# Kernel optimization log

Measured on AMD Instinct MI355X. Metric: run time of the kernel, lower is better.

## Reference

```python
import jax, jax.numpy as jnp
import numpy as np

B, S, D, H, L = 8, 2048, 512, 8, 5
DK = D // H
SP = S - L + 1  # number of local windows


def setup_inputs() -> dict:
    key = jax.random.key(0)
    ks = jax.random.split(key, 5)
    scale = 1.0 / np.sqrt(D).astype(np.float32)
    return {
        "query": jax.random.normal(ks[0], (B, S, D), dtype=jnp.float32),
        "key": jax.random.normal(ks[1], (B, S, D), dtype=jnp.float32),
        "value": jax.random.normal(ks[2], (B, S, D), dtype=jnp.float32),
        "W0": jax.random.normal(ks[3], (D, D), dtype=jnp.float32) * scale,
        "b0": jnp.zeros((D,), dtype=jnp.float32),
        "Wout": jax.random.normal(ks[4], (D, D), dtype=jnp.float32) * scale,
        "bout": jnp.zeros((D,), dtype=jnp.float32),
    }


def _local_agg(x, weighted):
    # x: (B, S, D). Sliding-window aggregation over windows of length L.
    # scores[b, t, s] = <x[b, t+L-1], x[b, s]> / sqrt(D)  -- per the source:
    # matmul(x[:, L-1:], x^T) / sqrt(d_model)
    scores = jnp.einsum("btd,bsd->bts", x[:, L - 1:], x) / (float(D) ** 0.5)
    idx = jnp.arange(SP)[:, None] + jnp.arange(L)[None, :]  # (SP, L)
    # per-window softmax over the L local scores
    w = jax.nn.softmax(jnp.take_along_axis(scores, idx[None, :, :], axis=-1), axis=-1)  # (B, SP, L)
    win = x[:, idx]  # (B, SP, L, D) gathered windows
    if weighted:
        win = w[..., None] * win
    return jnp.sum(win, axis=2)  # (B, SP, D)


def reference(query, key, value, W0, b0, Wout, bout):
    # Bug-faithful: the source overwrites the weighted query with the raw
    # windows (`query = q_list`), so query windows are summed UNweighted;
    # key windows use the local softmax weights.
    q = _local_agg(query, weighted=False)  # (B, SP, D)
    k = _local_agg(key, weighted=True)     # (B, SP, D)
    v = value[:, L - 1:] @ W0 + b0         # linears[0], aligned to SP positions

    def heads(t):  # (B, SP, D) -> (B, H, SP, DK)
        return t.reshape(t.shape[0], t.shape[1], H, DK).transpose(0, 2, 1, 3)

    qh, kh, vh = heads(q), heads(k), heads(v)
    att = jax.nn.softmax(jnp.einsum("bhtd,bhsd->bhts", qh, kh) / (float(DK) ** 0.5), axis=-1)
    x = jnp.einsum("bhts,bhsd->bhtd", att, vh)  # (B, H, SP, DK)
    x = x.transpose(0, 2, 1, 3).reshape(q.shape[0], SP, D)
    return x @ Wout + bout  # linears[-1]
```

## Files before the change

### kernel.cpp

```cpp
#include <hip/hip_runtime.h>
#include <hip/hip_bf16.h>
#include <hip/hip_fp16.h>

#define B_ 8
#define S_ 2048
#define D_ 512
#define H_ 8
#define L_ 5
#define DK_ 64
#define SP_ 2044
#define SPAD_ 2048

typedef _Float16 f16_t;
typedef _Float16 f16x4 __attribute__((ext_vector_type(4)));
typedef _Float16 f16x8 __attribute__((ext_vector_type(8)));
typedef __fp16 fp16x2_b __attribute__((ext_vector_type(2)));
typedef float f32x4 __attribute__((ext_vector_type(4)));
typedef float f32x16 __attribute__((ext_vector_type(16)));
typedef unsigned int u32;

static __device__ __forceinline__ f32x4 mfma16(f16x8 a, f16x8 b, f32x4 c) {
    return __builtin_amdgcn_mfma_f32_16x16x32_f16(a, b, c, 0, 0, 0);
}
static __device__ __forceinline__ f32x16 mfma32(f16x8 a, f16x8 b, f32x16 c) {
    return __builtin_amdgcn_mfma_f32_32x32x16_f16(a, b, c, 0, 0, 0);
}

union U32H2 { u32 u; fp16x2_b h; };
union FRAG { uint4 u; f16x8 f; };

#define LGKMBAR() do {                                 \
    __builtin_amdgcn_sched_barrier(0);                 \
    asm volatile("s_waitcnt lgkmcnt(0)");              \
    __builtin_amdgcn_s_barrier();                      \
    __builtin_amdgcn_sched_barrier(0);                 \
} while (0)

static __device__ __forceinline__ void swap32(u32 a, u32 b, u32& r0, u32& r1, int hi) {
#if __has_builtin(__builtin_amdgcn_permlane32_swap)
    auto r = __builtin_amdgcn_permlane32_swap(a, b, false, false);
    r0 = r[0]; r1 = r[1];
#else
    u32 t = __shfl_xor(hi ? a : b, 32, 64);
    r0 = hi ? t : a;
    r1 = hi ? b : t;
#endif
}

__global__ __launch_bounds__(256) void k_convert_w(
    const float* __restrict__ W0, const float* __restrict__ Wout,
    f16_t* __restrict__ WT0, f16_t* __restrict__ WT1) {
    int idx = blockIdx.x * 256 + threadIdx.x;
    int which = idx >> 18;
    int e = idx & 0x3FFFF;
    int k = e >> 9, n = e & 511;
    const float* W = which ? Wout : W0;
    f16_t* WT = which ? WT1 : WT0;
    WT[n * 512 + k] = (f16_t)W[k * 512 + n];
}

__global__ __launch_bounds__(256) void k_prep(
    const float* __restrict__ Qin, const float* __restrict__ Kin,
    f16_t* __restrict__ qh, f16_t* __restrict__ kh) {
    const int lane = threadIdx.x & 63;
    const int wid = threadIdx.x >> 6;
    const int gw = blockIdx.x * 4 + wid;
    const int b = gw >> 9;
    const int t0 = (gw & 511) * 4;
    const float* qb = Qin + (size_t)b * S_ * D_;
    const float* kb = Kin + (size_t)b * S_ * D_;
    const int d0 = lane * 8;

    float kr[8][8];
#pragma unroll
    for (int r = 0; r < 8; r++) {
        int row = t0 + r; row = row < 2047 ? row : 2047;
        const float4* kp = (const float4*)(kb + (size_t)row * D_ + d0);
        float4 ka = kp[0], kc = kp[1];
        kr[r][0] = ka.x; kr[r][1] = ka.y; kr[r][2] = ka.z; kr[r][3] = ka.w;
        kr[r][4] = kc.x; kr[r][5] = kc.y; kr[r][6] = kc.z; kr[r][7] = kc.w;
    }
    float qs[4][8];
#pragma unroll
    for (int w = 0; w < 4; w++)
#pragma unroll
        for (int e = 0; e < 8; e++) qs[w][e] = 0.f;
#pragma unroll
    for (int r = 0; r < 8; r++) {
        int row = t0 + r; row = row < 2047 ? row : 2047;
        const float4* qp = (const float4*)(qb + (size_t)row * D_ + d0);
        float4 a = qp[0], c = qp[1];
        float qe[8] = {a.x, a.y, a.z, a.w, c.x, c.y, c.z, c.w};
#pragma unroll
        for (int w = 0; w < 4; w++) {
            if (w <= r && r <= w + 4) {
#pragma unroll
                for (int e = 0; e < 8; e++) qs[w][e] += qe[e];
            }
        }
    }
    float dp[4][5];
#pragma unroll
    for (int w = 0; w < 4; w++) {
#pragma unroll
        for (int l = 0; l < 5; l++) {
            float d = 0.f;
#pragma unroll
            for (int e = 0; e < 8; e++) d += kr[w + 4][e] * kr[w + l][e];
            dp[w][l] = d;
        }
    }
#pragma unroll
    for (int m = 32; m; m >>= 1) {
#pragma unroll
        for (int w = 0; w < 4; w++)
#pragma unroll
            for (int l = 0; l < 5; l++) dp[w][l] += __shfl_xor(dp[w][l], m, 64);
    }
    const float sc = 0.044194173824159216f;
    const float qscale = 0.125f * 1.4426950408889634f;
    const int h = d0 >> 6, dk = d0 & 63;
#pragma unroll
    for (int w = 0; w < 4; w++) {
        float mx = dp[w][0];
#pragma unroll
        for (int l = 1; l < 5; l++) mx = fmaxf(mx, dp[w][l]);
        float wgt[5], sum = 0.f;
#pragma unroll
        for (int l = 0; l < 5; l++) { wgt[l] = __expf((dp[w][l] - mx) * sc); sum += wgt[l]; }
        float inv = 1.f / sum;
        f16x8 qpk, kpk;
#pragma unroll
        for (int e = 0; e < 8; e++) {
            float v = 0.f;
#pragma unroll
            for (int l = 0; l < 5; l++) v += wgt[l] * kr[w + l][e];
            kpk[e] = (f16_t)(v * inv);
            qpk[e] = (f16_t)(qs[w][e] * qscale);
        }
        const size_t ob = ((size_t)(b * H_ + h) * SPAD_ + (t0 + w)) * DK_ + dk;
        *(f16x8*)(qh + ob) = qpk;
        *(f16x8*)(kh + ob) = kpk;
    }
}

template <int MODE>
__global__ __launch_bounds__(256) void k_gemm(
    const void* __restrict__ Aptr, const f16_t* __restrict__ WT,
    const float* __restrict__ bias, void* __restrict__ Cptr) {
    __shared__ alignas(16) char smem[40960];
    const int tid = threadIdx.x, lane = tid & 63, wid = tid >> 6;
    const int mt = blockIdx.x >> 2, nt = blockIdx.x & 3;
    const int m0 = mt * 128, n0 = nt * 128;
    const int l15 = lane & 15, lg = lane >> 4;
    f32x4 acc[2][8] = {};

    const float* a0src = nullptr;
    const f16_t* a1src0 = nullptr, *a1src1 = nullptr;
    if (MODE == 0) {
        const float* A = (const float*)Aptr;
        int r = tid >> 1, cb = (tid & 1) * 16;
        int rp = m0 + r, b = rp >> 11, t = rp & 2047;
        int vrow = t + 4; vrow = vrow < 2047 ? vrow : 2047;
        a0src = A + ((size_t)b * 2048 + vrow) * 512 + cb;
    } else {
        const f16_t* A = (const f16_t*)Aptr;
        int r0 = tid >> 2, off0 = (tid & 3) * 8;
        int r1 = (tid + 256) >> 2;
        a1src0 = A + (size_t)(m0 + r0) * 512 + off0;
        a1src1 = A + (size_t)(m0 + r1) * 512 + off0;
    }
    const int bnl0 = tid >> 2, bko0 = (tid & 3) * 8;
    const int bnl1 = (tid + 256) >> 2;
    const f16_t* bsrc0 = WT + (size_t)(n0 + bnl0) * 512 + bko0;
    const f16_t* bsrc1 = WT + (size_t)(n0 + bnl1) * 512 + bko0;

    float4 fa[4];
    uint4 ua0, ua1, ub0, ub1;
    if (MODE == 0) {
#pragma unroll
        for (int j = 0; j < 4; j++) fa[j] = *(const float4*)(a0src + j * 4);
    } else {
        ua0 = *(const uint4*)a1src0;
        ua1 = *(const uint4*)a1src1;
    }
    ub0 = *(const uint4*)bsrc0;
    ub1 = *(const uint4*)bsrc1;

    for (int kt = 0; kt < 16; ++kt) {
        const int cur = kt & 1;
        f16_t (*Asm)[40] = (f16_t(*)[40])(smem + cur * 10240);
        f16_t (*Bsm)[40] = (f16_t(*)[40])(smem + 20480 + cur * 10240);
        if (MODE == 0) {
            int r = tid >> 1, cb = (tid & 1) * 16;
            f16x8 p0, p1;
            p0[0] = (f16_t)fa[0].x; p0[1] = (f16_t)fa[0].y; p0[2] = (f16_t)fa[0].z; p0[3] = (f16_t)fa[0].w;
            p0[4] = (f16_t)fa[1].x; p0[5] = (f16_t)fa[1].y; p0[6] = (f16_t)fa[1].z; p0[7] = (f16_t)fa[1].w;
            p1[0] = (f16_t)fa[2].x; p1[1] = (f16_t)fa[2].y; p1[2] = (f16_t)fa[2].z; p1[3] = (f16_t)fa[2].w;
            p1[4] = (f16_t)fa[3].x; p1[5] = (f16_t)fa[3].y; p1[6] = (f16_t)fa[3].z; p1[7] = (f16_t)fa[3].w;
            *(f16x8*)&Asm[r][cb] = p0;
            *(f16x8*)&Asm[r][cb + 8] = p1;
        } else {
            int r0 = tid >> 2, r1 = (tid + 256) >> 2, off = (tid & 3) * 8;
            *(uint4*)&Asm[r0][off] = ua0;
            *(uint4*)&Asm[r1][off] = ua1;
        }
        *(uint4*)&Bsm[bnl0][bko0] = ub0;
        *(uint4*)&Bsm[bnl1][bko0] = ub1;
        if (kt < 15) {
            const int k0n = (kt + 1) * 32;
            if (MODE == 0) {
#pragma unroll
                for (int j = 0; j < 4; j++) fa[j] = *(const float4*)(a0src + k0n + j * 4);
            } else {
                ua0 = *(const uint4*)(a1src0 + k0n);
                ua1 = *(const uint4*)(a1src1 + k0n);
            }
            ub0 = *(const uint4*)(bsrc0 + k0n);
            ub1 = *(const uint4*)(bsrc1 + k0n);
        }
        __syncthreads();
        f16x8 af[2], bfr[8];
#pragma unroll
        for (int i = 0; i < 2; i++) af[i] = *(const f16x8*)&Asm[wid * 32 + i * 16 + l15][lg * 8];
#pragma unroll
        for (int c = 0; c < 8; c++) bfr[c] = *(const f16x8*)&Bsm[c * 16 + l15][lg * 8];
        __builtin_amdgcn_s_setprio(1);
#pragma unroll
        for (int i = 0; i < 2; i++) {
#pragma unroll
            for (int c = 0; c < 8; c++) acc[i][c] = mfma16(af[i], bfr[c], acc[i][c]);
        }
        __builtin_amdgcn_s_setprio(0);
    }

    if (MODE == 0) {
        __syncthreads();
        f16_t (*Csm)[136] = (f16_t(*)[136])smem;
#pragma unroll
        for (int i = 0; i < 2; i++) {
#pragma unroll
            for (int c = 0; c < 8; c++) {
                int col = n0 + c * 16 + l15;
                float bv = bias[col];
                f16x4 pk;
#pragma unroll
                for (int r = 0; r < 4; r++) pk[r] = (f16_t)(acc[i][c][r] + bv);
                *(f16x4*)&Csm[c * 16 + l15][wid * 32 + i * 16 + lg * 4] = pk;
            }
        }
        __syncthreads();
        const int b = m0 >> 11, t0 = m0 & 2047;
        const int cl = tid >> 1, mo = (tid & 1) * 64;
        const int h = (n0 + cl) >> 6, dk = (n0 + cl) & 63;
        f16_t* dst = (f16_t*)Cptr + ((size_t)(b * H_ + h) * DK_ + dk) * SPAD_ + t0 + mo;
#pragma unroll
        for (int j = 0; j < 8; j++)
            *(uint4*)(dst + j * 8) = *(const uint4*)&Csm[cl][mo + j * 8];
    } else {
#pragma unroll
        for (int i = 0; i < 2; i++) {
#pragma unroll
            for (int c = 0; c < 8; c++) {
#pragma unroll
                for (int r = 0; r < 4; r++) {
                    int row = m0 + wid * 32 + i * 16 + lg * 4 + r;
                    int col = n0 + c * 16 + l15;
                    float v = acc[i][c][r] + bias[col];
                    int b = row >> 11, t = row & 2047;
                    if (t < SP_) {
                        float* outp = (float*)Cptr;
                        outp[((size_t)b * SP_ + t) * 512 + col] = v;
                    }
                }
            }
        }
    }
}

__global__ __launch_bounds__(256, 2) void k_attn(
    const f16_t* __restrict__ qh, const f16_t* __restrict__ kh,
    const f16_t* __restrict__ vhT, f16_t* __restrict__ xatt) {
    __shared__ alignas(16) f16_t Ksm[2][64][68];
    __shared__ alignas(16) f16_t Vsm[2][64][68];
    const int tid = threadIdx.x, lane = tid & 63, wid = tid >> 6;
    const int l31 = lane & 31, hi = lane >> 5, hi8 = hi * 8;
    const int vb = ((blockIdx.x & 7) << 6) | (blockIdx.x >> 3);
    const int bh = vb >> 3, qt = vb & 7;
    const f16_t* Q = qh + (size_t)bh * SPAD_ * DK_;
    const f16_t* K = kh + (size_t)bh * SPAD_ * DK_;
    const f16_t* VT = vhT + (size_t)bh * DK_ * SPAD_;
    const int qw = qt * 256 + wid * 64;

    f16x8 qf[2][4];
#pragma unroll
    for (int qg = 0; qg < 2; qg++)
#pragma unroll
        for (int kf = 0; kf < 4; kf++)
            qf[qg][kf] = *(const f16x8*)(Q + (size_t)(qw + qg * 32 + l31) * DK_ + kf * 16 + hi8);

    f32x16 cinit;
#pragma unroll
    for (int i = 0; i < 16; i++) cinit[i] = -12.f;

    f32x16 acc[2][2] = {};
    float rsa[2] = {0.f, 0.f}, rsb[2] = {0.f, 0.f};
    u32 pk[2][2][8];
    U32H2 one2; one2.u = 0x3C003C00u;

    const int sr = tid >> 3, so = (tid & 7) * 8;
    const f16_t* kg0 = K + (size_t)sr * DK_ + so;
    const f16_t* kg1 = K + (size_t)(sr + 32) * DK_ + so;
    const f16_t* vg0 = VT + (size_t)sr * SPAD_ + so;
    const f16_t* vg1 = VT + (size_t)(sr + 32) * SPAD_ + so;

    uint4 rk0 = *(const uint4*)kg0;
    uint4 rk1 = *(const uint4*)kg1;
    uint4 rv0 = *(const uint4*)vg0;
    uint4 rv1 = *(const uint4*)vg1;

    for (int t = 0; t < 32; ++t) {
        const int cur = t & 1;
        *(uint4*)&Ksm[cur][sr][so]      = rk0;
        *(uint4*)&Ksm[cur][sr + 32][so] = rk1;
        *(uint4*)&Vsm[cur][sr][so]      = rv0;
        *(uint4*)&Vsm[cur][sr + 32][so] = rv1;
        if (t < 31) {
            const int nxt = (t + 1) << 6;
            rk0 = *(const uint4*)(kg0 + (size_t)nxt * DK_);
            rk1 = *(const uint4*)(kg1 + (size_t)nxt * DK_);
            rv0 = *(const uint4*)(vg0 + nxt);
            rv1 = *(const uint4*)(vg1 + nxt);
        }
        LGKMBAR();

#pragma unroll
        for (int kr = 0; kr < 2; ++kr) {
            f32x16 sv0 = cinit, sv1 = cinit;
            __builtin_amdgcn_s_setprio(1);
#pragma unroll
            for (int kf = 0; kf < 4; ++kf) {
                f16x8 a = *(const f16x8*)&Ksm[cur][kr * 32 + l31][kf * 16 + hi8];
                sv0 = mfma32(a, qf[0][kf], sv0);
                sv1 = mfma32(a, qf[1][kf], sv1);
            }
            __builtin_amdgcn_s_setprio(0);
            if (t == 31 && kr == 1) {
#pragma unroll
                for (int r = 12; r < 16; ++r) {
                    sv0[r] = hi ? -1e30f : sv0[r];
                    sv1[r] = hi ? -1e30f : sv1[r];
                }
            }
#pragma unroll
            for (int j = 0; j < 8; ++j) {
                float a0 = __builtin_amdgcn_exp2f(sv0[2 * j]);
                float a1 = __builtin_amdgcn_exp2f(sv0[2 * j + 1]);
                U32H2 c0; c0.h = __builtin_amdgcn_cvt_pkrtz(a0, a1);
                pk[0][kr][j] = c0.u;
                float b0 = __builtin_amdgcn_exp2f(sv1[2 * j]);
                float b1 = __builtin_amdgcn_exp2f(sv1[2 * j + 1]);
                U32H2 c1; c1.h = __builtin_amdgcn_cvt_pkrtz(b0, b1);
                pk[1][kr][j] = c1.u;
#if __has_builtin(__builtin_amdgcn_fdot2)
                if (j & 1) {
                    rsb[0] = __builtin_amdgcn_fdot2(c0.h, one2.h, rsb[0], false);
                    rsb[1] = __builtin_amdgcn_fdot2(c1.h, one2.h, rsb[1], false);
                } else {
                    rsa[0] = __builtin_amdgcn_fdot2(c0.h, one2.h, rsa[0], false);
                    rsa[1] = __builtin_amdgcn_fdot2(c1.h, one2.h, rsa[1], false);
                }
#else
                if (j & 1) { rsb[0] += a0 + a1; rsb[1] += b0 + b1; }
                else       { rsa[0] += a0 + a1; rsa[1] += b0 + b1; }
#endif
            }
        }

#pragma unroll
        for (int kc = 0; kc < 4; ++kc) {
            const int kr = kc >> 1, al = (kc & 1) * 4;
            FRAG p0, p1;
            {
                u32 m0, m1, m2, m3;
                swap32(pk[0][kr][al],     pk[0][kr][al + 2], m0, m2, hi);
                swap32(pk[0][kr][al + 1], pk[0][kr][al + 3], m1, m3, hi);
                p0.u = make_uint4(m0, m1, m2, m3);
                swap32(pk[1][kr][al],     pk[1][kr][al + 2], m0, m2, hi);
                swap32(pk[1][kr][al + 1], pk[1][kr][al + 3], m1, m3, hi);
                p1.u = make_uint4(m0, m1, m2, m3);
            }
            __builtin_amdgcn_s_setprio(1);
#pragma unroll
            for (int dc = 0; dc < 2; ++dc) {
                f16x8 v = *(const f16x8*)&Vsm[cur][dc * 32 + l31][kc * 16 + hi8];
                acc[0][dc] = mfma32(v, p0.f, acc[0][dc]);
                acc[1][dc] = mfma32(v, p1.f, acc[1][dc]);
            }
            __builtin_amdgcn_s_setprio(0);
        }
    }

    float rs0 = rsa[0] + rsb[0];
    float rs1 = rsa[1] + rsb[1];
    rs0 += __shfl_xor(rs0, 32, 64);
    rs1 += __shfl_xor(rs1, 32, 64);
    const float inv[2] = {1.f / rs0, 1.f / rs1};

    __syncthreads();
    f16_t (*Osm)[68] = (f16_t(*)[68])&Ksm[0][0][0];
#pragma unroll
    for (int qg = 0; qg < 2; ++qg) {
        const int row = wid * 64 + qg * 32 + l31;
#pragma unroll
        for (int dc = 0; dc < 2; ++dc) {
#pragma unroll
            for (int p = 0; p < 8; ++p) {
                float e0 = acc[qg][dc][2 * p] * inv[qg];
                float e1 = acc[qg][dc][2 * p + 1] * inv[qg];
                U32H2 c; c.h = __builtin_amdgcn_cvt_pkrtz(e0, e1);
                const int d = dc * 32 + 2 * (p & 1) + 8 * (p >> 1) + 4 * hi;
                *(u32*)&Osm[row][d] = c.u;
            }
        }
    }
    __syncthreads();
    const int b = bh >> 3, hh = bh & 7;
#pragma unroll
    for (int ps = 0; ps < 8; ++ps) {
        const int row = wid * 64 + ps * 8 + (lane >> 3);
        const int dco = (lane & 7) * 8;
        uint4 v = *(const uint4*)&Osm[row][dco];
        f16_t* dst = xatt + ((size_t)b * SPAD_ + qt * 256 + row) * D_ + hh * DK_ + dco;
        *(uint4*)dst = v;
    }
}

extern "C" void kernel_launch(void* const* d_in, const int* in_sizes, int n_in,
                              void* d_out, int out_size, void* d_ws, size_t ws_size,
                              hipStream_t stream) {
    const float* query = (const float*)d_in[0];
    const float* key   = (const float*)d_in[1];
    const float* value = (const float*)d_in[2];
    const float* W0    = (const float*)d_in[3];
    const float* b0    = (const float*)d_in[4];
    const float* Wout  = (const float*)d_in[5];
    const float* bout  = (const float*)d_in[6];
    float* out = (float*)d_out;

    char* w = (char*)d_ws;
    const size_t SZ = (size_t)B_ * H_ * SPAD_ * DK_ * sizeof(f16_t);
    f16_t* qh   = (f16_t*)w; w += SZ;
    f16_t* kh   = (f16_t*)w; w += SZ;
    f16_t* vhT  = (f16_t*)w; w += SZ;
    f16_t* xatt = (f16_t*)w; w += SZ;
    f16_t* WT0  = (f16_t*)w; w += (size_t)512 * 512 * sizeof(f16_t);
    f16_t* WT1  = (f16_t*)w; w += (size_t)512 * 512 * sizeof(f16_t);

    k_convert_w<<<2048, 256, 0, stream>>>(W0, Wout, WT0, WT1);
    k_prep<<<1024, 256, 0, stream>>>(query, key, qh, kh);
    k_gemm<0><<<512, 256, 0, stream>>>((const void*)value, WT0, b0, (void*)vhT);
    k_attn<<<512, 256, 0, stream>>>(qh, kh, vhT, xatt);
    k_gemm<1><<<512, 256, 0, stream>>>((const void*)xatt, WT1, bout, (void*)out);
}
```

Before: 150.9 us.

## Merge value GEMM with local-window prep into one launch; tile weight transpose

Combines the V projection GEMM and the query/key sliding-window prep into a single kernel. The first 512 blocks run the GEMM and the remaining 1024 run the prep, so the two independent stages overlap and one launch disappears. The weight transpose/convert kernel now stages 64x64 tiles through shared memory, giving coalesced reads and vectorized writes in place of strided scattered writes. The combined kernel uses the larger shared-memory footprint for every block, including prep blocks that do not need it, which may lower their occupancy.

```diff
diff --git a/kernel.cpp b/kernel.cpp
--- a/kernel.cpp
+++ b/kernel.cpp
@@ -50,104 +50,210 @@
 __global__ __launch_bounds__(256) void k_convert_w(
     const float* __restrict__ W0, const float* __restrict__ Wout,
     f16_t* __restrict__ WT0, f16_t* __restrict__ WT1) {
-    int idx = blockIdx.x * 256 + threadIdx.x;
-    int which = idx >> 18;
-    int e = idx & 0x3FFFF;
-    int k = e >> 9, n = e & 511;
+    __shared__ float T[64][65];
+    const int bid = blockIdx.x;
+    const int which = bid >> 6;
+    const int tile = bid & 63;
+    const int K0 = (tile >> 3) * 64, N0 = (tile & 7) * 64;
     const float* W = which ? Wout : W0;
     f16_t* WT = which ? WT1 : WT0;
-    WT[n * 512 + k] = (f16_t)W[k * 512 + n];
-}
-
-__global__ __launch_bounds__(256) void k_prep(
+    const int t = threadIdx.x;
+    const int r = t >> 2, c4 = (t & 3) * 16;
+    const float4* src = (const float4*)(W + (size_t)(K0 + r) * 512 + N0 + c4);
+#pragma unroll
+    for (int j = 0; j < 4; j++) {
+        float4 v = src[j];
+        T[r][c4 + 4 * j + 0] = v.x; T[r][c4 + 4 * j + 1] = v.y;
+        T[r][c4 + 4 * j + 2] = v.z; T[r][c4 + 4 * j + 3] = v.w;
+    }
+    __syncthreads();
+    const int n = t >> 2, k4 = (t & 3) * 16;
+    f16_t outv[16];
+#pragma unroll
+    for (int j = 0; j < 16; j++) outv[j] = (f16_t)T[k4 + j][n];
+    f16_t* dst = WT + (size_t)(N0 + n) * 512 + K0 + k4;
+    *(uint4*)dst = *(uint4*)&outv[0];
+    *(uint4*)(dst + 8) = *(uint4*)&outv[8];
+}
+
+__global__ __launch_bounds__(256) void k_pg(
     const float* __restrict__ Qin, const float* __restrict__ Kin,
-    f16_t* __restrict__ qh, f16_t* __restrict__ kh) {
-    const int lane = threadIdx.x & 63;
-    const int wid = threadIdx.x >> 6;
-    const int gw = blockIdx.x * 4 + wid;
-    const int b = gw >> 9;
-    const int t0 = (gw & 511) * 4;
-    const float* qb = Qin + (size_t)b * S_ * D_;
-    const float* kb = Kin + (size_t)b * S_ * D_;
-    const int d0 = lane * 8;
-
-    float kr[8][8];
-#pragma unroll
-    for (int r = 0; r < 8; r++) {
-        int row = t0 + r; row = row < 2047 ? row : 2047;
-        const float4* kp = (const float4*)(kb + (size_t)row * D_ + d0);
-        float4 ka = kp[0], kc = kp[1];
-        kr[r][0] = ka.x; kr[r][1] = ka.y; kr[r][2] = ka.z; kr[r][3] = ka.w;
-        kr[r][4] = kc.x; kr[r][5] = kc.y; kr[r][6] = kc.z; kr[r][7] = kc.w;
-    }
-    float qs[4][8];
-#pragma unroll
-    for (int w = 0; w < 4; w++)
-#pragma unroll
-        for (int e = 0; e < 8; e++) qs[w][e] = 0.f;
-#pragma unroll
-    for (int r = 0; r < 8; r++) {
-        int row = t0 + r; row = row < 2047 ? row : 2047;
-        const float4* qp = (const float4*)(qb + (size_t)row * D_ + d0);
-        float4 a = qp[0], c = qp[1];
-        float qe[8] = {a.x, a.y, a.z, a.w, c.x, c.y, c.z, c.w};
+    f16_t* __restrict__ qh, f16_t* __restrict__ kh,
+    const float* __restrict__ Vin, const f16_t* __restrict__ WT0,
+    const float* __restrict__ b0, f16_t* __restrict__ vhT) {
+    __shared__ alignas(16) char smem[40960];
+    const int tid = threadIdx.x, lane = tid & 63, wid = tid >> 6;
+
+    if (blockIdx.x < 512) {
+        const int mt = blockIdx.x >> 2, nt = blockIdx.x & 3;
+        const int m0 = mt * 128, n0 = nt * 128;
+        const int l15 = lane & 15, lg = lane >> 4;
+        f32x4 acc[2][8] = {};
+
+        const float* a0src;
+        {
+            int r = tid >> 1, cb = (tid & 1) * 16;
+            int rp = m0 + r, b = rp >> 11, t = rp & 2047;
+            int vrow = t + 4; vrow = vrow < 2047 ? vrow : 2047;
+            a0src = Vin + ((size_t)b * 2048 + vrow) * 512 + cb;
+        }
+        const int bnl0 = tid >> 2, bko0 = (tid & 3) * 8;
+        const int bnl1 = (tid + 256) >> 2;
+        const f16_t* bsrc0 = WT0 + (size_t)(n0 + bnl0) * 512 + bko0;
+        const f16_t* bsrc1 = WT0 + (size_t)(n0 + bnl1) * 512 + bko0;
+
+        float4 fa[4];
+        uint4 ub0, ub1;
+#pragma unroll
+        for (int j = 0; j < 4; j++) fa[j] = *(const float4*)(a0src + j * 4);
+        ub0 = *(const uint4*)bsrc0;
+        ub1 = *(const uint4*)bsrc1;
+
+        for (int kt = 0; kt < 16; ++kt) {
+            const int cur = kt & 1;
+            f16_t (*Asm)[40] = (f16_t(*)[40])(smem + cur * 10240);
+            f16_t (*Bsm)[40] = (f16_t(*)[40])(smem + 20480 + cur * 10240);
+            {
+                int r = tid >> 1, cb = (tid & 1) * 16;
+                f16x8 p0, p1;
+                p0[0] = (f16_t)fa[0].x; p0[1] = (f16_t)fa[0].y; p0[2] = (f16_t)fa[0].z; p0[3] = (f16_t)fa[0].w;
+                p0[4] = (f16_t)fa[1].x; p0[5] = (f16_t)fa[1].y; p0[6] = (f16_t)fa[1].z; p0[7] = (f16_t)fa[1].w;
+                p1[0] = (f16_t)fa[2].x; p1[1] = (f16_t)fa[2].y; p1[2] = (f16_t)fa[2].z; p1[3] = (f16_t)fa[2].w;
+                p1[4] = (f16_t)fa[3].x; p1[5] = (f16_t)fa[3].y; p1[6] = (f16_t)fa[3].z; p1[7] = (f16_t)fa[3].w;
+                *(f16x8*)&Asm[r][cb] = p0;
+                *(f16x8*)&Asm[r][cb + 8] = p1;
+            }
+            *(uint4*)&Bsm[bnl0][bko0] = ub0;
+            *(uint4*)&Bsm[bnl1][bko0] = ub1;
+            if (kt < 15) {
+                const int k0n = (kt + 1) * 32;
+#pragma unroll
+                for (int j = 0; j < 4; j++) fa[j] = *(const float4*)(a0src + k0n + j * 4);
+                ub0 = *(const uint4*)(bsrc0 + k0n);
+                ub1 = *(const uint4*)(bsrc1 + k0n);
+            }
+            __syncthreads();
+            f16x8 af[2], bfr[8];
+#pragma unroll
+            for (int i = 0; i < 2; i++) af[i] = *(const f16x8*)&Asm[wid * 32 + i * 16 + l15][lg * 8];
+#pragma unroll
+            for (int c = 0; c < 8; c++) bfr[c] = *(const f16x8*)&Bsm[c * 16 + l15][lg * 8];
+            __builtin_amdgcn_s_setprio(1);
+#pragma unroll
+            for (int i = 0; i < 2; i++) {
+#pragma unroll
+                for (int c = 0; c < 8; c++) acc[i][c] = mfma16(af[i], bfr[c], acc[i][c]);
+            }
+            __builtin_amdgcn_s_setprio(0);
+        }
+
+        __syncthreads();
+        f16_t (*Csm)[136] = (f16_t(*)[136])smem;
+#pragma unroll
+        for (int i = 0; i < 2; i++) {
+#pragma unroll
+            for (int c = 0; c < 8; c++) {
+                int col = n0 + c * 16 + l15;
+                float bv = b0[col];
+                f16x4 pk;
+#pragma unroll
+                for (int r = 0; r < 4; r++) pk[r] = (f16_t)(acc[i][c][r] + bv);
+                *(f16x4*)&Csm[c * 16 + l15][wid * 32 + i * 16 + lg * 4] = pk;
+            }
+        }
+        __syncthreads();
+        const int b = m0 >> 11, t0 = m0 & 2047;
+        const int cl = tid >> 1, mo = (tid & 1) * 64;
+        const int h = (n0 + cl) >> 6, dk = (n0 + cl) & 63;
+        f16_t* dst = vhT + ((size_t)(b * H_ + h) * DK_ + dk) * SPAD_ + t0 + mo;
+#pragma unroll
+        for (int j = 0; j < 8; j++)
+            *(uint4*)(dst + j * 8) = *(const uint4*)&Csm[cl][mo + j * 8];
+    } else {
+        const int gw = (blockIdx.x - 512) * 4 + wid;
+        const int b = gw >> 9;
+        const int t0 = (gw & 511) * 4;
+        const float* qb = Qin + (size_t)b * S_ * D_;
+        const float* kb = Kin + (size_t)b * S_ * D_;
+        const int d0 = lane * 8;
+
+        float kr[8][8];
+#pragma unroll
+        for (int r = 0; r < 8; r++) {
+            int row = t0 + r; row = row < 2047 ? row : 2047;
+            const float4* kp = (const float4*)(kb + (size_t)row * D_ + d0);
+            float4 ka = kp[0], kc = kp[1];
+            kr[r][0] = ka.x; kr[r][1] = ka.y; kr[r][2] = ka.z; kr[r][3] = ka.w;
+            kr[r][4] = kc.x; kr[r][5] = kc.y; kr[r][6] = kc.z; kr[r][7] = kc.w;
+        }
+        float qs[4][8];
+#pragma unroll
+        for (int w = 0; w < 4; w++)
+#pragma unroll
+            for (int e = 0; e < 8; e++) qs[w][e] = 0.f;
+#pragma unroll
+        for (int r = 0; r < 8; r++) {
+            int row = t0 + r; row = row < 2047 ? row : 2047;
+            const float4* qp = (const float4*)(qb + (size_t)row * D_ + d0);
+            float4 a = qp[0], c = qp[1];
+            float qe[8] = {a.x, a.y, a.z, a.w, c.x, c.y, c.z, c.w};
+#pragma unroll
+            for (int w = 0; w < 4; w++) {
+                if (w <= r && r <= w + 4) {
+#pragma unroll
+                    for (int e = 0; e < 8; e++) qs[w][e] += qe[e];
+                }
+            }
+        }
+        float dp[4][5];
 #pragma unroll
         for (int w = 0; w < 4; w++) {
-            if (w <= r && r <= w + 4) {
-#pragma unroll
-                for (int e = 0; e < 8; e++) qs[w][e] += qe[e];
-            }
-        }
-    }
-    float dp[4][5];
-#pragma unroll
-    for (int w = 0; w < 4; w++) {
-#pragma unroll
-        for (int l = 0; l < 5; l++) {
-            float d = 0.f;
-#pragma unroll
-            for (int e = 0; e < 8; e++) d += kr[w + 4][e] * kr[w + l][e];
-            dp[w][l] = d;
-        }
-    }
-#pragma unroll
-    for (int m = 32; m; m >>= 1) {
-#pragma unroll
-        for (int w = 0; w < 4; w++)
-#pragma unroll
-            for (int l = 0; l < 5; l++) dp[w][l] += __shfl_xor(dp[w][l], m, 64);
-    }
-    const float sc = 0.044194173824159216f;
-    const float qscale = 0.125f * 1.4426950408889634f;
-    const int h = d0 >> 6, dk = d0 & 63;
-#pragma unroll
-    for (int w = 0; w < 4; w++) {
-        float mx = dp[w][0];
-#pragma unroll
-        for (int l = 1; l < 5; l++) mx = fmaxf(mx, dp[w][l]);
-        float wgt[5], sum = 0.f;
-#pragma unroll
-        for (int l = 0; l < 5; l++) { wgt[l] = __expf((dp[w][l] - mx) * sc); sum += wgt[l]; }
-        float inv = 1.f / sum;
-        f16x8 qpk, kpk;
-#pragma unroll
-        for (int e = 0; e < 8; e++) {
-            float v = 0.f;
-#pragma unroll
-            for (int l = 0; l < 5; l++) v += wgt[l] * kr[w + l][e];
-            kpk[e] = (f16_t)(v * inv);
-            qpk[e] = (f16_t)(qs[w][e] * qscale);
-        }
-        const size_t ob = ((size_t)(b * H_ + h) * SPAD_ + (t0 + w)) * DK_ + dk;
-        *(f16x8*)(qh + ob) = qpk;
-        *(f16x8*)(kh + ob) = kpk;
-    }
-}
-
-template <int MODE>
-__global__ __launch_bounds__(256) void k_gemm(
-    const void* __restrict__ Aptr, const f16_t* __restrict__ WT,
-    const float* __restrict__ bias, void* __restrict__ Cptr) {
+#pragma unroll
+            for (int l = 0; l < 5; l++) {
+                float d = 0.f;
+#pragma unroll
+                for (int e = 0; e < 8; e++) d += kr[w + 4][e] * kr[w + l][e];
+                dp[w][l] = d;
+            }
+        }
+#pragma unroll
+        for (int m = 32; m; m >>= 1) {
+#pragma unroll
+            for (int w = 0; w < 4; w++)
+#pragma unroll
+                for (int l = 0; l < 5; l++) dp[w][l] += __shfl_xor(dp[w][l], m, 64);
+        }
+        const float sc = 0.044194173824159216f;
+        const float qscale = 0.125f * 1.4426950408889634f;
+        const int h = d0 >> 6, dk = d0 & 63;
+#pragma unroll
+        for (int w = 0; w < 4; w++) {
+            float mx = dp[w][0];
+#pragma unroll
+            for (int l = 1; l < 5; l++) mx = fmaxf(mx, dp[w][l]);
+            float wgt[5], sum = 0.f;
+#pragma unroll
+            for (int l = 0; l < 5; l++) { wgt[l] = __expf((dp[w][l] - mx) * sc); sum += wgt[l]; }
+            float inv = 1.f / sum;
+            f16x8 qpk, kpk;
+#pragma unroll
+            for (int e = 0; e < 8; e++) {
+                float v = 0.f;
+#pragma unroll
+                for (int l = 0; l < 5; l++) v += wgt[l] * kr[w + l][e];
+                kpk[e] = (f16_t)(v * inv);
+                qpk[e] = (f16_t)(qs[w][e] * qscale);
+            }
+            const size_t ob = ((size_t)(b * H_ + h) * SPAD_ + (t0 + w)) * DK_ + dk;
+            *(f16x8*)(qh + ob) = qpk;
+            *(f16x8*)(kh + ob) = kpk;
+        }
+    }
+}
+
+__global__ __launch_bounds__(256) void k_gemm1(
+    const f16_t* __restrict__ A, const f16_t* __restrict__ WT,
+    const float* __restrict__ bias, float* __restrict__ outp) {
     __shared__ alignas(16) char smem[40960];
     const int tid = threadIdx.x, lane = tid & 63, wid = tid >> 6;
     const int mt = blockIdx.x >> 2, nt = blockIdx.x & 3;
@@ -155,67 +261,32 @@
     const int l15 = lane & 15, lg = lane >> 4;
     f32x4 acc[2][8] = {};
 
-    const float* a0src = nullptr;
-    const f16_t* a1src0 = nullptr, *a1src1 = nullptr;
-    if (MODE == 0) {
-        const float* A = (const float*)Aptr;
-        int r = tid >> 1, cb = (tid & 1) * 16;
-        int rp = m0 + r, b = rp >> 11, t = rp & 2047;
-        int vrow = t + 4; vrow = vrow < 2047 ? vrow : 2047;
-        a0src = A + ((size_t)b * 2048 + vrow) * 512 + cb;
-    } else {
-        const f16_t* A = (const f16_t*)Aptr;
-        int r0 = tid >> 2, off0 = (tid & 3) * 8;
-        int r1 = (tid + 256) >> 2;
-        a1src0 = A + (size_t)(m0 + r0) * 512 + off0;
-        a1src1 = A + (size_t)(m0 + r1) * 512 + off0;
-    }
+    const int r0i = tid >> 2, off0 = (tid & 3) * 8;
+    const int r1i = (tid + 256) >> 2;
+    const f16_t* a1src0 = A + (size_t)(m0 + r0i) * 512 + off0;
+    const f16_t* a1src1 = A + (size_t)(m0 + r1i) * 512 + off0;
     const int bnl0 = tid >> 2, bko0 = (tid & 3) * 8;
     const int bnl1 = (tid + 256) >> 2;
     const f16_t* bsrc0 = WT + (size_t)(n0 + bnl0) * 512 + bko0;
     const f16_t* bsrc1 = WT + (size_t)(n0 + bnl1) * 512 + bko0;
 
-    float4 fa[4];
-    uint4 ua0, ua1, ub0, ub1;
-    if (MODE == 0) {
-#pragma unroll
-        for (int j = 0; j < 4; j++) fa[j] = *(const float4*)(a0src + j * 4);
-    } else {
-        ua0 = *(const uint4*)a1src0;
-        ua1 = *(const uint4*)a1src1;
-    }
-    ub0 = *(const uint4*)bsrc0;
-    ub1 = *(const uint4*)bsrc1;
+    uint4 ua0 = *(const uint4*)a1src0;
+    uint4 ua1 = *(const uint4*)a1src1;
+    uint4 ub0 = *(const uint4*)bsrc0;
+    uint4 ub1 = *(const uint4*)bsrc1;
 
     for (int kt = 0; kt < 16; ++kt) {
         const int cur = kt & 1;
         f16_t (*Asm)[40] = (f16_t(*)[40])(smem + cur * 10240);
         f16_t (*Bsm)[40] = (f16_t(*)[40])(smem + 20480 + cur * 10240);
-        if (MODE == 0) {
-            int r = tid >> 1, cb = (tid & 1) * 16;
-            f16x8 p0, p1;
-            p0[0] = (f16_t)fa[0].x; p0[1] = (f16_t)fa[0].y; p0[2] = (f16_t)fa[0].z; p0[3] = (f16_t)fa[0].w;
-            p0[4] = (f16_t)fa[1].x; p0[5] = (f16_t)fa[1].y; p0[6] = (f16_t)fa[1].z; p0[7] = (f16_t)fa[1].w;
-            p1[0] = (f16_t)fa[2].x; p1[1] = (f16_t)fa[2].y; p1[2] = (f16_t)fa[2].z; p1[3] = (f16_t)fa[2].w;
-            p1[4] = (f16_t)fa[3].x; p1[5] = (f16_t)fa[3].y; p1[6] = (f16_t)fa[3].z; p1[7] = (f16_t)fa[3].w;
-            *(f16x8*)&Asm[r][cb] = p0;
-            *(f16x8*)&Asm[r][cb + 8] = p1;
-        } else {
-            int r0 = tid >> 2, r1 = (tid + 256) >> 2, off = (tid & 3) * 8;
-            *(uint4*)&Asm[r0][off] = ua0;
-            *(uint4*)&Asm[r1][off] = ua1;
-        }
+        *(uint4*)&Asm[r0i][off0] = ua0;
+        *(uint4*)&Asm[r1i][off0] = ua1;
         *(uint4*)&Bsm[bnl0][bko0] = ub0;
         *(uint4*)&Bsm[bnl1][bko0] = ub1;
         if (kt < 15) {
             const int k0n = (kt + 1) * 32;
-            if (MODE == 0) {
-#pragma unroll
-                for (int j = 0; j < 4; j++) fa[j] = *(const float4*)(a0src + k0n + j * 4);
-            } else {
-                ua0 = *(const uint4*)(a1src0 + k0n);
-                ua1 = *(const uint4*)(a1src1 + k0n);
-            }
+            ua0 = *(const uint4*)(a1src0 + k0n);
+            ua1 = *(const uint4*)(a1src1 + k0n);
             ub0 = *(const uint4*)(bsrc0 + k0n);
             ub1 = *(const uint4*)(bsrc1 + k0n);
         }
@@ -234,44 +305,18 @@
         __builtin_amdgcn_s_setprio(0);
     }
 
-    if (MODE == 0) {
-        __syncthreads();
-        f16_t (*Csm)[136] = (f16_t(*)[136])smem;
-#pragma unroll
-        for (int i = 0; i < 2; i++) {
-#pragma unroll
-            for (int c = 0; c < 8; c++) {
+#pragma unroll
+    for (int i = 0; i < 2; i++) {
+#pragma unroll
+        for (int c = 0; c < 8; c++) {
+#pragma unroll
+            for (int r = 0; r < 4; r++) {
+                int row = m0 + wid * 32 + i * 16 + lg * 4 + r;
                 int col = n0 + c * 16 + l15;
-                float bv = bias[col];
-                f16x4 pk;
-#pragma unroll
-                for (int r = 0; r < 4; r++) pk[r] = (f16_t)(acc[i][c][r] + bv);
-                *(f16x4*)&Csm[c * 16 + l15][wid * 32 + i * 16 + lg * 4] = pk;
-            }
-        }
-        __syncthreads();
-        const int b = m0 >> 11, t0 = m0 & 2047;
-        const int cl = tid >> 1, mo = (tid & 1) * 64;
-        const int h = (n0 + cl) >> 6, dk = (n0 + cl) & 63;
-        f16_t* dst = (f16_t*)Cptr + ((size_t)(b * H_ + h) * DK_ + dk) * SPAD_ + t0 + mo;
-#pragma unroll
-        for (int j = 0; j < 8; j++)
-            *(uint4*)(dst + j * 8) = *(const uint4*)&Csm[cl][mo + j * 8];
-    } else {
-#pragma unroll
-        for (int i = 0; i < 2; i++) {
-#pragma unroll
-            for (int c = 0; c < 8; c++) {
-#pragma unroll
-                for (int r = 0; r < 4; r++) {
-                    int row = m0 + wid * 32 + i * 16 + lg * 4 + r;
-                    int col = n0 + c * 16 + l15;
-                    float v = acc[i][c][r] + bias[col];
-                    int b = row >> 11, t = row & 2047;
-                    if (t < SP_) {
-                        float* outp = (float*)Cptr;
-                        outp[((size_t)b * SP_ + t) * 512 + col] = v;
-                    }
+                float v = acc[i][c][r] + bias[col];
+                int b = row >> 11, t = row & 2047;
+                if (t < SP_) {
+                    outp[((size_t)b * SP_ + t) * 512 + col] = v;
                 }
             }
         }
@@ -457,9 +502,8 @@
     f16_t* WT0  = (f16_t*)w; w += (size_t)512 * 512 * sizeof(f16_t);
     f16_t* WT1  = (f16_t*)w; w += (size_t)512 * 512 * sizeof(f16_t);
 
-    k_convert_w<<<2048, 256, 0, stream>>>(W0, Wout, WT0, WT1);
-    k_prep<<<1024, 256, 0, stream>>>(query, key, qh, kh);
-    k_gemm<0><<<512, 256, 0, stream>>>((const void*)value, WT0, b0, (void*)vhT);
+    k_convert_w<<<128, 256, 0, stream>>>(W0, Wout, WT0, WT1);
+    k_pg<<<1536, 256, 0, stream>>>(query, key, qh, kh, value, WT0, b0, vhT);
     k_attn<<<512, 256, 0, stream>>>(qh, kh, vhT, xatt);
-    k_gemm<1><<<512, 256, 0, stream>>>((const void*)xatt, WT1, bout, (void*)out);
-}
+    k_gemm1<<<512, 256, 0, stream>>>(xatt, WT1, bout, out);
+}
```

After: 145.5 us. -3.6%, faster.
